# Kernel tuning notes

Hardware: AMD Instinct MI355X
Metric: run time of the kernel (lower is better)

## Reference

```python
import jax, jax.numpy as jnp
import numpy as np

D_MODEL = 1024
N_HEADS = 16
DEPTH = D_MODEL // N_HEADS
B, S = 2, 2048


def layer_norm(x, gamma, beta):
    # Faithful to the torch module: unbiased std (ddof=1), eps added to std.
    mean = jnp.mean(x, axis=-1, keepdims=True)
    std = jnp.std(x, axis=-1, ddof=1, keepdims=True)
    return gamma * ((x - mean) / (std + 1e-6)) + beta


def setup_inputs() -> dict:
    key = jax.random.key(0)
    ks = jax.random.split(key, 12)
    sc = 0.02
    x = jax.random.normal(ks[0], (B, S, D_MODEL), jnp.float32)
    mask = jnp.triu(jnp.ones((S, S), jnp.float32), k=1)  # 1 where masked (future)
    return {
        "x": x,
        "mask": mask,
        "wq_w": jax.random.normal(ks[1], (D_MODEL, D_MODEL), jnp.float32) * sc,
        "wq_b": jnp.zeros((D_MODEL,), jnp.float32),
        "wk_w": jax.random.normal(ks[2], (D_MODEL, D_MODEL), jnp.float32) * sc,
        "wk_b": jnp.zeros((D_MODEL,), jnp.float32),
        "wv_w": jax.random.normal(ks[3], (D_MODEL, D_MODEL), jnp.float32) * sc,
        "wv_b": jnp.zeros((D_MODEL,), jnp.float32),
        "dense_w": jax.random.normal(ks[4], (D_MODEL, D_MODEL), jnp.float32) * sc,
        "dense_b": jnp.zeros((D_MODEL,), jnp.float32),
        "gamma1": jnp.ones((D_MODEL,), jnp.float32),
        "beta1": jnp.zeros((D_MODEL,), jnp.float32),
        "gamma2": jnp.ones((D_MODEL,), jnp.float32),
        "beta2": jnp.zeros((D_MODEL,), jnp.float32),
        "fc_w": jax.random.normal(ks[5], (4 * D_MODEL, D_MODEL), jnp.float32) * sc,
        "proj_w": jax.random.normal(ks[6], (D_MODEL, 4 * D_MODEL), jnp.float32) * sc,
    }


def reference(x, mask, wq_w, wq_b, wk_w, wk_b, wv_w, wv_b, dense_w, dense_b,
              gamma1, beta1, gamma2, beta2, fc_w, proj_w):
    # x: [B,S,D]. Dropout is identity in eval.
    xn = layer_norm(x, gamma1, beta1)

    def split(h):  # [B,S,D] -> [B,H,S,depth]
        return h.reshape(B, S, N_HEADS, DEPTH).transpose(0, 2, 1, 3)

    q = split(xn @ wq_w.T + wq_b)
    k = split(xn @ wk_w.T + wk_b)
    v = split(xn @ wv_w.T + wv_b)

    scores = jnp.einsum("bhqd,bhkd->bhqk", q, k) / jnp.sqrt(
        jnp.asarray(DEPTH, jnp.float32))
    scores = scores + mask * -1e9
    attn = jax.nn.softmax(scores, axis=-1)
    ctx = jnp.einsum("bhqk,bhkd->bhqd", attn, v)
    ctx = ctx.transpose(0, 2, 1, 3).reshape(B, S, D_MODEL)
    attn_out = ctx @ dense_w.T + dense_b

    # Residual adds the *normed* x (faithful to the original ordering).
    h = xn + attn_out
    hn = layer_norm(h, gamma2, beta2)

    ff = jax.nn.gelu(hn @ fc_w.T, approximate=False) @ proj_w.T
    return hn + ff
```

## Files before the change

kernel.cpp:

```cpp
#include <hip/hip_runtime.h>
#include <math.h>

typedef __bf16 bf16;
typedef __attribute__((ext_vector_type(2))) __bf16 bf16x2;
typedef __attribute__((ext_vector_type(4))) __bf16 bf16x4;
typedef __attribute__((ext_vector_type(8))) __bf16 bf16x8;
typedef __attribute__((ext_vector_type(4))) float f32x4;

#define D_MODEL 1024
#define NH 16
#define DP 64
#define BB 2
#define SEQ 2048
#define TOK 4096
#define FFD 4096
#define AST 72

__device__ __forceinline__ void async16(bf16* lds, const bf16* g) {
    __builtin_amdgcn_global_load_lds(
        (__attribute__((address_space(1))) void*)g,
        (__attribute__((address_space(3))) void*)lds, 16, 0, 0);
}

__device__ __forceinline__ f32x4 mfma16(bf16x8 a, bf16x8 b, f32x4 c) {
    return __builtin_amdgcn_mfma_f32_16x16x32_bf16(a, b, c, 0, 0, 0);
}

struct CvtArgs {
    const float4* in[6];
    bf16x4* out[6];
};
__global__ __launch_bounds__(256) void cvt_all(CvtArgs a)
{
    const int i = blockIdx.x * 256 + threadIdx.x;
    int seg, idx;
    if (i < (1 << 20)) { seg = i >> 18; idx = i & ((1 << 18) - 1); }
    else {
        const int j = i - (1 << 20);
        seg = 4 + (j >> 20); idx = j & ((1 << 20) - 1);
    }
    const float4 v = a.in[seg][idx];
    bf16x4 o; o[0] = (bf16)v.x; o[1] = (bf16)v.y; o[2] = (bf16)v.z; o[3] = (bf16)v.w;
    a.out[seg][idx] = o;
}

template<typename TIN>
__global__ __launch_bounds__(256) void ln_kernel(
    const TIN* __restrict__ in, const float* __restrict__ g,
    const float* __restrict__ be, bf16* __restrict__ out)
{
    const size_t row = blockIdx.x;
    const int t = threadIdx.x;
    const TIN* x = in + row * D_MODEL;

    float v0, v1, v2, v3;
    if constexpr (sizeof(TIN) == 4) {
        const float4 xv = *(const float4*)(x + t * 4);
        v0 = xv.x; v1 = xv.y; v2 = xv.z; v3 = xv.w;
    } else {
        const bf16x4 xv = *(const bf16x4*)(x + t * 4);
        v0 = (float)xv[0]; v1 = (float)xv[1]; v2 = (float)xv[2]; v3 = (float)xv[3];
    }
    float s  = v0 + v1 + v2 + v3;
    float ss = v0*v0 + v1*v1 + v2*v2 + v3*v3;
    #pragma unroll
    for (int off = 32; off > 0; off >>= 1) {
        s  += __shfl_down(s, off);
        ss += __shfl_down(ss, off);
    }
    __shared__ float rs[4], rss[4];
    if ((t & 63) == 0) { rs[t >> 6] = s; rss[t >> 6] = ss; }
    __syncthreads();
    const float S  = rs[0] + rs[1] + rs[2] + rs[3];
    const float SS = rss[0] + rss[1] + rss[2] + rss[3];
    const float mean = S * (1.0f / 1024.0f);
    const float var  = fmaxf((SS - S * mean) * (1.0f / 1023.0f), 0.0f);
    const float inv  = 1.0f / (sqrtf(var) + 1e-6f);

    const float4 gv = *(const float4*)(g  + t * 4);
    const float4 bv = *(const float4*)(be + t * 4);
    bf16x4 ov;
    ov[0] = (bf16)(gv.x * ((v0 - mean) * inv) + bv.x);
    ov[1] = (bf16)(gv.y * ((v1 - mean) * inv) + bv.y);
    ov[2] = (bf16)(gv.z * ((v2 - mean) * inv) + bv.z);
    ov[3] = (bf16)(gv.w * ((v3 - mean) * inv) + bv.w);
    *(bf16x4*)(out + row * D_MODEL + t * 4) = ov;
}

template<int EPI, typename TOUT>
__global__ __launch_bounds__(256, 2) void gemm_bt(
    const bf16* __restrict__ A, const bf16* __restrict__ W,
    const float* __restrict__ bias, const bf16* res,
    TOUT* C, int M, int N, int K, float scale)
{
    __shared__ __align__(16) bf16 As[2][128 * 32];
    __shared__ __align__(16) bf16 Bs[2][128 * 32];
    const int t = threadIdx.x;
    const int w = t >> 6, lane = t & 63;
    const int fr = lane & 15, quad = lane >> 4;
    const int m0 = blockIdx.y * 128, n0 = blockIdx.x * 128;
    const int wm = (w >> 1) * 64, wn = (w & 1) * 64;

    const f32x4 z = {0.f, 0.f, 0.f, 0.f};
    f32x4 acc[4][4];
    #pragma unroll
    for (int i = 0; i < 4; ++i)
        #pragma unroll
        for (int j = 0; j < 4; ++j) acc[i][j] = z;

    const int nk = K >> 5;
    const int srow = t >> 2, ssub = t & 3;

    #pragma unroll
    for (int call = 0; call < 2; ++call) {
        const int row = call * 64 + srow;
        async16(&As[0][(size_t)(call * 256 + w * 64) * 8],
                A + (size_t)(m0 + row) * K + ssub * 8);
        async16(&Bs[0][(size_t)(call * 256 + w * 64) * 8],
                W + (size_t)(n0 + row) * K + ssub * 8);
    }
    __syncthreads();

    for (int kt = 0; kt < nk; ++kt) {
        const int cur = kt & 1;
        if (kt + 1 < nk) {
            const int k0 = (kt + 1) << 5;
            #pragma unroll
            for (int call = 0; call < 2; ++call) {
                const int row = call * 64 + srow;
                async16(&As[cur ^ 1][(size_t)(call * 256 + w * 64) * 8],
                        A + (size_t)(m0 + row) * K + k0 + ssub * 8);
                async16(&Bs[cur ^ 1][(size_t)(call * 256 + w * 64) * 8],
                        W + (size_t)(n0 + row) * K + k0 + ssub * 8);
            }
        }
        bf16x8 af[4], bfr[4];
        #pragma unroll
        for (int i = 0; i < 4; ++i)
            af[i] = *(const bf16x8*)&As[cur][(wm + i * 16 + fr) * 32 + quad * 8];
        #pragma unroll
        for (int j = 0; j < 4; ++j)
            bfr[j] = *(const bf16x8*)&Bs[cur][(wn + j * 16 + fr) * 32 + quad * 8];
        #pragma unroll
        for (int i = 0; i < 4; ++i)
            #pragma unroll
            for (int j = 0; j < 4; ++j)
                acc[i][j] = mfma16(af[i], bfr[j], acc[i][j]);
        __syncthreads();
    }

    #pragma unroll
    for (int i = 0; i < 4; ++i) {
        #pragma unroll
        for (int j = 0; j < 4; ++j) {
            #pragma unroll
            for (int r = 0; r < 4; ++r) {
                const int m = m0 + wm + i * 16 + quad * 4 + r;
                const int n = n0 + wn + j * 16 + fr;
                float v = acc[i][j][r];
                if (EPI == 1) {
                    v += bias[n];
                    v += (float)res[(size_t)m * N + n];
                    C[(size_t)m * N + n] = (TOUT)v;
                } else if (EPI == 2) {
                    v = 0.5f * v * (1.0f + erff(v * 0.70710678118f));
                    C[(size_t)m * N + n] = (TOUT)v;
                } else {
                    v += (float)res[(size_t)m * N + n];
                    C[(size_t)m * N + n] = (TOUT)v;
                }
            }
        }
    }
}

template<int EPI, typename TOUT>
__global__ __launch_bounds__(256, 2) void gemm_bt64(
    const bf16* __restrict__ A, const bf16* __restrict__ W,
    const float* __restrict__ bias, const bf16* res,
    TOUT* C, int M, int N, int K)
{
    __shared__ __align__(16) bf16 As[2][128 * 32];
    __shared__ __align__(16) bf16 Bs[2][64 * 32];
    const int t = threadIdx.x;
    const int w = t >> 6, lane = t & 63;
    const int fr = lane & 15, quad = lane >> 4;
    const int m0 = blockIdx.y * 128, n0 = blockIdx.x * 64;
    const int wm = (w >> 1) * 64, wn = (w & 1) * 32;

    const f32x4 z = {0.f, 0.f, 0.f, 0.f};
    f32x4 acc[4][2];
    #pragma unroll
    for (int i = 0; i < 4; ++i)
        #pragma unroll
        for (int j = 0; j < 2; ++j) acc[i][j] = z;

    const int nk = K >> 5;
    const int srow = t >> 2, ssub = t & 3;

    #pragma unroll
    for (int call = 0; call < 2; ++call) {
        const int row = call * 64 + srow;
        async16(&As[0][(size_t)(call * 256 + w * 64) * 8],
                A + (size_t)(m0 + row) * K + ssub * 8);
    }
    async16(&Bs[0][(size_t)(w * 64) * 8],
            W + (size_t)(n0 + srow) * K + ssub * 8);
    __syncthreads();

    for (int kt = 0; kt < nk; ++kt) {
        const int cur = kt & 1;
        if (kt + 1 < nk) {
            const int k0 = (kt + 1) << 5;
            #pragma unroll
            for (int call = 0; call < 2; ++call) {
                const int row = call * 64 + srow;
                async16(&As[cur ^ 1][(size_t)(call * 256 + w * 64) * 8],
                        A + (size_t)(m0 + row) * K + k0 + ssub * 8);
            }
            async16(&Bs[cur ^ 1][(size_t)(w * 64) * 8],
                    W + (size_t)(n0 + srow) * K + k0 + ssub * 8);
        }
        bf16x8 af[4], bfr[2];
        #pragma unroll
        for (int i = 0; i < 4; ++i)
            af[i] = *(const bf16x8*)&As[cur][(wm + i * 16 + fr) * 32 + quad * 8];
        #pragma unroll
        for (int j = 0; j < 2; ++j)
            bfr[j] = *(const bf16x8*)&Bs[cur][(wn + j * 16 + fr) * 32 + quad * 8];
        #pragma unroll
        for (int i = 0; i < 4; ++i)
            #pragma unroll
            for (int j = 0; j < 2; ++j)
                acc[i][j] = mfma16(af[i], bfr[j], acc[i][j]);
        __syncthreads();
    }

    #pragma unroll
    for (int i = 0; i < 4; ++i) {
        #pragma unroll
        for (int j = 0; j < 2; ++j) {
            #pragma unroll
            for (int r = 0; r < 4; ++r) {
                const int m = m0 + wm + i * 16 + quad * 4 + r;
                const int n = n0 + wn + j * 16 + fr;
                float v = acc[i][j][r];
                if (EPI == 1) {
                    v += bias[n];
                    v += (float)res[(size_t)m * N + n];
                    C[(size_t)m * N + n] = (TOUT)v;
                } else {
                    v += (float)res[(size_t)m * N + n];
                    C[(size_t)m * N + n] = (TOUT)v;
                }
            }
        }
    }
}

__global__ __launch_bounds__(256, 2) void gemm_qkv(
    const bf16* __restrict__ A,
    const bf16* __restrict__ wq, const bf16* __restrict__ wk,
    const bf16* __restrict__ wvv,
    const float* __restrict__ bq, const float* __restrict__ bk,
    const float* __restrict__ bv,
    bf16* __restrict__ outq, bf16* __restrict__ outk, bf16* __restrict__ outv)
{
    const int sel = blockIdx.x >> 3;
    const bf16* W = (sel == 0) ? wq : ((sel == 1) ? wk : wvv);
    const float* bias = (sel == 0) ? bq : ((sel == 1) ? bk : bv);
    bf16* C = (sel == 0) ? outq : ((sel == 1) ? outk : outv);
    const float scale = (sel == 0) ? 0.125f : 1.0f;
    const int K = D_MODEL;

    __shared__ __align__(16) bf16 As[2][128 * 32];
    __shared__ __align__(16) bf16 Bs[2][128 * 32];
    const int t = threadIdx.x;
    const int w = t >> 6, lane = t & 63;
    const int fr = lane & 15, quad = lane >> 4;
    const int m0 = blockIdx.y * 128, n0 = (blockIdx.x & 7) * 128;
    const int wm = (w >> 1) * 64, wn = (w & 1) * 64;

    const f32x4 z = {0.f, 0.f, 0.f, 0.f};
    f32x4 acc[4][4];
    #pragma unroll
    for (int i = 0; i < 4; ++i)
        #pragma unroll
        for (int j = 0; j < 4; ++j) acc[i][j] = z;

    const int nk = D_MODEL >> 5;
    const int srow = t >> 2, ssub = t & 3;

    #pragma unroll
    for (int call = 0; call < 2; ++call) {
        const int row = call * 64 + srow;
        async16(&As[0][(size_t)(call * 256 + w * 64) * 8],
                A + (size_t)(m0 + row) * K + ssub * 8);
        async16(&Bs[0][(size_t)(call * 256 + w * 64) * 8],
                W + (size_t)(n0 + row) * K + ssub * 8);
    }
    __syncthreads();

    for (int kt = 0; kt < nk; ++kt) {
        const int cur = kt & 1;
        if (kt + 1 < nk) {
            const int k0 = (kt + 1) << 5;
            #pragma unroll
            for (int call = 0; call < 2; ++call) {
                const int row = call * 64 + srow;
                async16(&As[cur ^ 1][(size_t)(call * 256 + w * 64) * 8],
                        A + (size_t)(m0 + row) * K + k0 + ssub * 8);
                async16(&Bs[cur ^ 1][(size_t)(call * 256 + w * 64) * 8],
                        W + (size_t)(n0 + row) * K + k0 + ssub * 8);
            }
        }
        bf16x8 af[4], bfr[4];
        #pragma unroll
        for (int i = 0; i < 4; ++i)
            af[i] = *(const bf16x8*)&As[cur][(wm + i * 16 + fr) * 32 + quad * 8];
        #pragma unroll
        for (int j = 0; j < 4; ++j)
            bfr[j] = *(const bf16x8*)&Bs[cur][(wn + j * 16 + fr) * 32 + quad * 8];
        #pragma unroll
        for (int i = 0; i < 4; ++i)
            #pragma unroll
            for (int j = 0; j < 4; ++j)
                acc[i][j] = mfma16(af[i], bfr[j], acc[i][j]);
        __syncthreads();
    }

    #pragma unroll
    for (int i = 0; i < 4; ++i)
        #pragma unroll
        for (int j = 0; j < 4; ++j)
            #pragma unroll
            for (int r = 0; r < 4; ++r) {
                const int m = m0 + wm + i * 16 + quad * 4 + r;
                const int n = n0 + wn + j * 16 + fr;
                const float vv = (acc[i][j][r] + bias[n]) * scale;
                const int b = m >> 11, s = m & 2047, h = n >> 6, d = n & 63;
                C[(((size_t)(b * NH + h)) * SEQ + s) * DP + d] = (bf16)vv;
            }
}

__global__ __launch_bounds__(256, 2) void attn_kernel(
    const bf16* __restrict__ q, const bf16* __restrict__ k,
    const bf16* __restrict__ v, bf16* __restrict__ ctx)
{
    __shared__ __align__(16) bf16 Ks[2][64 * AST];
    __shared__ __align__(16) bf16 VsT[2][64 * AST];
    __shared__ __align__(16) bf16 Ps[4][16 * AST];
    const int t = threadIdx.x, wv = t >> 6, lane = t & 63;
    const int fr = lane & 15, quad = lane >> 4;
    const int bh = blockIdx.y;
    const size_t base = (size_t)bh * SEQ * DP;
    const int b = bh >> 4, hh = bh & 15;
    const f32x4 z = {0.f, 0.f, 0.f, 0.f};
    const int krow = t >> 2, kd0 = (t & 3) * 16;
    const int pp = t & 31, c0 = (t >> 5) * 8;

    for (int half = 0; half < 2; ++half) {
        const int qt = half ? (31 - (int)blockIdx.x) : (int)blockIdx.x;
        const int q0 = qt * 64, qr0 = q0 + wv * 16;
        const int nkt = qt + 1;

        __syncthreads();

        bf16x8 qf[2];
        #pragma unroll
        for (int c = 0; c < 2; ++c)
            qf[c] = *(const bf16x8*)(q + base + (size_t)(qr0 + fr) * DP + c * 32 + quad * 8);

        bf16x8 k0r, k1r, v0r, v1r;
        {
            const bf16* kp = k + base + (size_t)krow * DP + kd0;
            k0r = *(const bf16x8*)kp; k1r = *(const bf16x8*)(kp + 8);
            const bf16* vp = v + base + (size_t)(2 * pp) * DP + c0;
            v0r = *(const bf16x8*)vp; v1r = *(const bf16x8*)(vp + DP);
        }

        f32x4 o[4] = {z, z, z, z};
        float mi[4] = {-1e30f, -1e30f, -1e30f, -1e30f};
        float li[4] = {0.f, 0.f, 0.f, 0.f};

        for (int kt = 0; kt < nkt; ++kt) {
            const int cur = kt & 1;
            const int kk0 = kt * 64;
            *(bf16x8*)&Ks[cur][krow * AST + kd0]     = k0r;
            *(bf16x8*)&Ks[cur][krow * AST + kd0 + 8] = k1r;
            #pragma unroll
            for (int j = 0; j < 8; ++j) {
                bf16x2 pr; pr[0] = v0r[j]; pr[1] = v1r[j];
                *(bf16x2*)&VsT[cur][(c0 + j) * AST + 2 * pp] = pr;
            }
            __syncthreads();
            if (kt + 1 < nkt) {
                const bf16* kp = k + base + (size_t)(kk0 + 64 + krow) * DP + kd0;
                k0r = *(const bf16x8*)kp; k1r = *(const bf16x8*)(kp + 8);
                const bf16* vp = v + base + (size_t)(kk0 + 64 + 2 * pp) * DP + c0;
                v0r = *(const bf16x8*)vp; v1r = *(const bf16x8*)(vp + DP);
            }

            f32x4 sa[4] = {z, z, z, z};
            #pragma unroll
            for (int nb = 0; nb < 4; ++nb)
                #pragma unroll
                for (int c = 0; c < 2; ++c) {
                    const bf16x8 kf = *(const bf16x8*)&Ks[cur][(nb * 16 + fr) * AST + c * 32 + quad * 8];
                    sa[nb] = mfma16(qf[c], kf, sa[nb]);
                }

            float p[4][4], rmax[4];
            #pragma unroll
            for (int r = 0; r < 4; ++r) rmax[r] = -1e30f;
            #pragma unroll
            for (int nb = 0; nb < 4; ++nb)
                #pragma unroll
                for (int r = 0; r < 4; ++r) {
                    const int key = kk0 + nb * 16 + fr;
                    const int qrow = qr0 + quad * 4 + r;
                    float sv = sa[nb][r];
                    if (key > qrow) sv += -1e9f;
                    p[nb][r] = sv;
                    rmax[r] = fmaxf(rmax[r], sv);
                }
            #pragma unroll
            for (int off = 1; off < 16; off <<= 1)
                #pragma unroll
                for (int r = 0; r < 4; ++r)
                    rmax[r] = fmaxf(rmax[r], __shfl_xor(rmax[r], off));

            float alpha[4], psum[4];
            #pragma unroll
            for (int r = 0; r < 4; ++r) {
                const float nm = fmaxf(mi[r], rmax[r]);
                alpha[r] = __expf(mi[r] - nm);
                mi[r] = nm;
                float ps = 0.f;
                #pragma unroll
                for (int nb = 0; nb < 4; ++nb) {
                    const float e = __expf(p[nb][r] - nm);
                    p[nb][r] = e;
                    ps += e;
                }
                psum[r] = ps;
            }
            #pragma unroll
            for (int off = 1; off < 16; off <<= 1)
                #pragma unroll
                for (int r = 0; r < 4; ++r)
                    psum[r] += __shfl_xor(psum[r], off);
            #pragma unroll
            for (int r = 0; r < 4; ++r) li[r] = li[r] * alpha[r] + psum[r];
            #pragma unroll
            for (int db = 0; db < 4; ++db)
                #pragma unroll
                for (int r = 0; r < 4; ++r) o[db][r] *= alpha[r];

            #pragma unroll
            for (int nb = 0; nb < 4; ++nb)
                #pragma unroll
                for (int r = 0; r < 4; ++r)
                    Ps[wv][(quad * 4 + r) * AST + nb * 16 + fr] = (bf16)p[nb][r];

            bf16x8 pf[2];
            #pragma unroll
            for (int c = 0; c < 2; ++c)
                pf[c] = *(const bf16x8*)&Ps[wv][fr * AST + c * 32 + quad * 8];
            #pragma unroll
            for (int db = 0; db < 4; ++db)
                #pragma unroll
                for (int c = 0; c < 2; ++c) {
                    const bf16x8 vf = *(const bf16x8*)&VsT[cur][(db * 16 + fr) * AST + c * 32 + quad * 8];
                    o[db] = mfma16(pf[c], vf, o[db]);
                }
        }

        #pragma unroll
        for (int db = 0; db < 4; ++db)
            #pragma unroll
            for (int r = 0; r < 4; ++r) {
                const int qrow = qr0 + quad * 4 + r;
                const int d = db * 16 + fr;
                ctx[((size_t)(b * SEQ + qrow)) * D_MODEL + hh * DP + d] =
                    (bf16)(o[db][r] / li[r]);
            }
    }
}

extern "C" void kernel_launch(void* const* d_in, const int* in_sizes, int n_in,
                              void* d_out, int out_size, void* d_ws, size_t ws_size,
                              hipStream_t stream) {
    const float* x       = (const float*)d_in[0];
    const float* wq_w    = (const float*)d_in[2];
    const float* wq_b    = (const float*)d_in[3];
    const float* wk_w    = (const float*)d_in[4];
    const float* wk_b    = (const float*)d_in[5];
    const float* wv_w    = (const float*)d_in[6];
    const float* wv_b    = (const float*)d_in[7];
    const float* dense_w = (const float*)d_in[8];
    const float* dense_b = (const float*)d_in[9];
    const float* gamma1  = (const float*)d_in[10];
    const float* beta1   = (const float*)d_in[11];
    const float* gamma2  = (const float*)d_in[12];
    const float* beta2   = (const float*)d_in[13];
    const float* fc_w    = (const float*)d_in[14];
    const float* proj_w  = (const float*)d_in[15];
    float* out = (float*)d_out;

    bf16* ws = (bf16*)d_ws;
    const size_t M1 = (size_t)1 << 20;
    bf16* xn   = ws;
    bf16* qb   = ws + 4 * M1;
    bf16* kb   = ws + 8 * M1;
    bf16* vb   = ws + 12 * M1;
    bf16* ctx  = ws + 16 * M1;
    bf16* ff1  = qb;
    bf16* wqc  = ws + 20 * M1;
    bf16* wkc  = ws + 21 * M1;
    bf16* wvc  = ws + 22 * M1;
    bf16* wdc  = ws + 23 * M1;
    bf16* fcc  = ws + 24 * M1;
    bf16* prjc = ws + 28 * M1;
    bf16* h = xn, *hn = xn;

    CvtArgs ca;
    ca.in[0] = (const float4*)wq_w;    ca.out[0] = (bf16x4*)wqc;
    ca.in[1] = (const float4*)wk_w;    ca.out[1] = (bf16x4*)wkc;
    ca.in[2] = (const float4*)wv_w;    ca.out[2] = (bf16x4*)wvc;
    ca.in[3] = (const float4*)dense_w; ca.out[3] = (bf16x4*)wdc;
    ca.in[4] = (const float4*)fc_w;    ca.out[4] = (bf16x4*)fcc;
    ca.in[5] = (const float4*)proj_w;  ca.out[5] = (bf16x4*)prjc;
    cvt_all<<<12288, 256, 0, stream>>>(ca);

    ln_kernel<float><<<TOK, 256, 0, stream>>>(x, gamma1, beta1, xn);
    gemm_qkv<<<dim3(24, 32), 256, 0, stream>>>(xn, wqc, wkc, wvc,
                                               wq_b, wk_b, wv_b, qb, kb, vb);
    attn_kernel<<<dim3(16, BB * NH), 256, 0, stream>>>(qb, kb, vb, ctx);
    gemm_bt64<1, bf16><<<dim3(16, 32), 256, 0, stream>>>(ctx, wdc, dense_b, xn, h,
                                                         TOK, D_MODEL, D_MODEL);
    ln_kernel<bf16><<<TOK, 256, 0, stream>>>(h, gamma2, beta2, hn);
    gemm_bt<2, bf16><<<dim3(32, 32), 256, 0, stream>>>(hn, fcc, nullptr, nullptr, ff1,
                                                       TOK, FFD, D_MODEL, 1.0f);
    gemm_bt64<3, float><<<dim3(16, 32), 256, 0, stream>>>(ff1, prjc, nullptr, hn, out,
                                                          TOK, D_MODEL, FFD);
}
```

Baseline: 388.8 us.

## Add XCD-aware block swizzle, split-K final projection, and MFMA priority hints

Remaps workgroup indices in the GEMMs and the attention kernel so consecutive tiles land on the same XCD, which should improve L2 reuse of shared operand tiles. The final FFN projection (K=4096) is split into two K-halves across gridDim.z, writing fp32 partials that a new combine kernel sums with the residual. This doubles the grid to fill more CUs. Attention also raises wave priority around the MFMA blocks. Costs are an extra partial buffer round-trip and one more launch, and the partial buffer reuses workspace that previously held the converted weights, which is only safe because those weights are dead by then.

```diff
diff --git a/kernel.cpp b/kernel.cpp
--- a/kernel.cpp
+++ b/kernel.cpp
@@ -26,6 +26,18 @@
     return __builtin_amdgcn_mfma_f32_16x16x32_bf16(a, b, c, 0, 0, 0);
 }
 
+__device__ __forceinline__ void xcd_swz(int& bx, int& by, int& bz) {
+    const int gx = gridDim.x, gy = gridDim.y;
+    const int nwg = gx * gy * gridDim.z;
+    const int orig = (blockIdx.z * gy + blockIdx.y) * gx + blockIdx.x;
+    const int q = nwg >> 3;
+    const int n = (orig & 7) * q + (orig >> 3);
+    bx = n % gx;
+    const int r = n / gx;
+    by = r % gy;
+    bz = r / gy;
+}
+
 struct CvtArgs {
     const float4* in[6];
     bf16x4* out[6];
@@ -93,12 +105,13 @@
     const float* __restrict__ bias, const bf16* res,
     TOUT* C, int M, int N, int K, float scale)
 {
+    int bx, by, bz; xcd_swz(bx, by, bz);
     __shared__ __align__(16) bf16 As[2][128 * 32];
     __shared__ __align__(16) bf16 Bs[2][128 * 32];
     const int t = threadIdx.x;
     const int w = t >> 6, lane = t & 63;
     const int fr = lane & 15, quad = lane >> 4;
-    const int m0 = blockIdx.y * 128, n0 = blockIdx.x * 128;
+    const int m0 = by * 128, n0 = bx * 128;
     const int wm = (w >> 1) * 64, wn = (w & 1) * 64;
 
     const f32x4 z = {0.f, 0.f, 0.f, 0.f};
@@ -178,14 +191,17 @@
 __global__ __launch_bounds__(256, 2) void gemm_bt64(
     const bf16* __restrict__ A, const bf16* __restrict__ W,
     const float* __restrict__ bias, const bf16* res,
-    TOUT* C, int M, int N, int K)
-{
+    TOUT* C, TOUT* Cb, int M, int N, int K, int kchunk)
+{
+    int bx, by, bz; xcd_swz(bx, by, bz);
     __shared__ __align__(16) bf16 As[2][128 * 32];
     __shared__ __align__(16) bf16 Bs[2][64 * 32];
     const int t = threadIdx.x;
     const int w = t >> 6, lane = t & 63;
     const int fr = lane & 15, quad = lane >> 4;
-    const int m0 = blockIdx.y * 128, n0 = blockIdx.x * 64;
+    const int m0 = by * 128, n0 = bx * 64;
+    const int kbase = bz * kchunk;
+    TOUT* Cz = (EPI == 4 && bz) ? Cb : C;
     const int wm = (w >> 1) * 64, wn = (w & 1) * 32;
 
     const f32x4 z = {0.f, 0.f, 0.f, 0.f};
@@ -195,23 +211,23 @@
         #pragma unroll
         for (int j = 0; j < 2; ++j) acc[i][j] = z;
 
-    const int nk = K >> 5;
+    const int nk = kchunk >> 5;
     const int srow = t >> 2, ssub = t & 3;
 
     #pragma unroll
     for (int call = 0; call < 2; ++call) {
         const int row = call * 64 + srow;
         async16(&As[0][(size_t)(call * 256 + w * 64) * 8],
-                A + (size_t)(m0 + row) * K + ssub * 8);
+                A + (size_t)(m0 + row) * K + kbase + ssub * 8);
     }
     async16(&Bs[0][(size_t)(w * 64) * 8],
-            W + (size_t)(n0 + srow) * K + ssub * 8);
+            W + (size_t)(n0 + srow) * K + kbase + ssub * 8);
     __syncthreads();
 
     for (int kt = 0; kt < nk; ++kt) {
         const int cur = kt & 1;
         if (kt + 1 < nk) {
-            const int k0 = (kt + 1) << 5;
+            const int k0 = kbase + ((kt + 1) << 5);
             #pragma unroll
             for (int call = 0; call < 2; ++call) {
                 const int row = call * 64 + srow;
@@ -248,14 +264,31 @@
                 if (EPI == 1) {
                     v += bias[n];
                     v += (float)res[(size_t)m * N + n];
-                    C[(size_t)m * N + n] = (TOUT)v;
+                    Cz[(size_t)m * N + n] = (TOUT)v;
+                } else if (EPI == 4) {
+                    Cz[(size_t)m * N + n] = (TOUT)v;
                 } else {
                     v += (float)res[(size_t)m * N + n];
-                    C[(size_t)m * N + n] = (TOUT)v;
+                    Cz[(size_t)m * N + n] = (TOUT)v;
                 }
             }
         }
     }
+}
+
+__global__ __launch_bounds__(256) void combine_add(
+    const float4* __restrict__ p1, const bf16x4* __restrict__ res,
+    float4* __restrict__ out)
+{
+    const int i = blockIdx.x * 256 + threadIdx.x;
+    const float4 a = out[i], b = p1[i];
+    const bf16x4 r = res[i];
+    float4 o;
+    o.x = a.x + b.x + (float)r[0];
+    o.y = a.y + b.y + (float)r[1];
+    o.z = a.z + b.z + (float)r[2];
+    o.w = a.w + b.w + (float)r[3];
+    out[i] = o;
 }
 
 __global__ __launch_bounds__(256, 2) void gemm_qkv(
@@ -266,7 +299,8 @@
     const float* __restrict__ bv,
     bf16* __restrict__ outq, bf16* __restrict__ outk, bf16* __restrict__ outv)
 {
-    const int sel = blockIdx.x >> 3;
+    int bx, by, bz; xcd_swz(bx, by, bz);
+    const int sel = bx >> 3;
     const bf16* W = (sel == 0) ? wq : ((sel == 1) ? wk : wvv);
     const float* bias = (sel == 0) ? bq : ((sel == 1) ? bk : bv);
     bf16* C = (sel == 0) ? outq : ((sel == 1) ? outk : outv);
@@ -278,7 +312,7 @@
     const int t = threadIdx.x;
     const int w = t >> 6, lane = t & 63;
     const int fr = lane & 15, quad = lane >> 4;
-    const int m0 = blockIdx.y * 128, n0 = (blockIdx.x & 7) * 128;
+    const int m0 = by * 128, n0 = (bx & 7) * 128;
     const int wm = (w >> 1) * 64, wn = (w & 1) * 64;
 
     const f32x4 z = {0.f, 0.f, 0.f, 0.f};
@@ -352,7 +386,10 @@
     __shared__ __align__(16) bf16 Ps[4][16 * AST];
     const int t = threadIdx.x, wv = t >> 6, lane = t & 63;
     const int fr = lane & 15, quad = lane >> 4;
-    const int bh = blockIdx.y;
+    const int id = blockIdx.y * 16 + blockIdx.x;
+    const int nid = (id & 7) * 64 + (id >> 3);
+    const int bh = nid >> 4;
+    const int qxi = nid & 15;
     const size_t base = (size_t)bh * SEQ * DP;
     const int b = bh >> 4, hh = bh & 15;
     const f32x4 z = {0.f, 0.f, 0.f, 0.f};
@@ -360,7 +397,7 @@
     const int pp = t & 31, c0 = (t >> 5) * 8;
 
     for (int half = 0; half < 2; ++half) {
-        const int qt = half ? (31 - (int)blockIdx.x) : (int)blockIdx.x;
+        const int qt = half ? (31 - qxi) : qxi;
         const int q0 = qt * 64, qr0 = q0 + wv * 16;
         const int nkt = qt + 1;
 
@@ -402,6 +439,7 @@
             }
 
             f32x4 sa[4] = {z, z, z, z};
+            __builtin_amdgcn_s_setprio(1);
             #pragma unroll
             for (int nb = 0; nb < 4; ++nb)
                 #pragma unroll
@@ -409,6 +447,7 @@
                     const bf16x8 kf = *(const bf16x8*)&Ks[cur][(nb * 16 + fr) * AST + c * 32 + quad * 8];
                     sa[nb] = mfma16(qf[c], kf, sa[nb]);
                 }
+            __builtin_amdgcn_s_setprio(0);
 
             float p[4][4], rmax[4];
             #pragma unroll
@@ -467,6 +506,7 @@
             #pragma unroll
             for (int c = 0; c < 2; ++c)
                 pf[c] = *(const bf16x8*)&Ps[wv][fr * AST + c * 32 + quad * 8];
+            __builtin_amdgcn_s_setprio(1);
             #pragma unroll
             for (int db = 0; db < 4; ++db)
                 #pragma unroll
@@ -474,6 +514,7 @@
                     const bf16x8 vf = *(const bf16x8*)&VsT[cur][(db * 16 + fr) * AST + c * 32 + quad * 8];
                     o[db] = mfma16(pf[c], vf, o[db]);
                 }
+            __builtin_amdgcn_s_setprio(0);
         }
 
         #pragma unroll
@@ -523,6 +564,7 @@
     bf16* fcc  = ws + 24 * M1;
     bf16* prjc = ws + 28 * M1;
     bf16* h = xn, *hn = xn;
+    float* part1 = (float*)(ws + 20 * M1);
 
     CvtArgs ca;
     ca.in[0] = (const float4*)wq_w;    ca.out[0] = (bf16x4*)wqc;
@@ -537,11 +579,13 @@
     gemm_qkv<<<dim3(24, 32), 256, 0, stream>>>(xn, wqc, wkc, wvc,
                                                wq_b, wk_b, wv_b, qb, kb, vb);
     attn_kernel<<<dim3(16, BB * NH), 256, 0, stream>>>(qb, kb, vb, ctx);
-    gemm_bt64<1, bf16><<<dim3(16, 32), 256, 0, stream>>>(ctx, wdc, dense_b, xn, h,
-                                                         TOK, D_MODEL, D_MODEL);
+    gemm_bt64<1, bf16><<<dim3(16, 32), 256, 0, stream>>>(
+        ctx, wdc, dense_b, xn, h, (bf16*)nullptr, TOK, D_MODEL, D_MODEL, D_MODEL);
     ln_kernel<bf16><<<TOK, 256, 0, stream>>>(h, gamma2, beta2, hn);
     gemm_bt<2, bf16><<<dim3(32, 32), 256, 0, stream>>>(hn, fcc, nullptr, nullptr, ff1,
                                                        TOK, FFD, D_MODEL, 1.0f);
-    gemm_bt64<3, float><<<dim3(16, 32), 256, 0, stream>>>(ff1, prjc, nullptr, hn, out,
-                                                          TOK, D_MODEL, FFD);
-}
+    gemm_bt64<4, float><<<dim3(16, 32, 2), 256, 0, stream>>>(
+        ff1, prjc, nullptr, nullptr, out, part1, TOK, D_MODEL, FFD, FFD / 2);
+    combine_add<<<4096, 256, 0, stream>>>(
+        (const float4*)part1, (const bf16x4*)hn, (float4*)out);
+}
```

Result: no change. 382.0 us (-1.7%).
